# Kernel tuning notes

Measured on AMD Instinct MI355X. Metric: run time of the kernel, lower is better.

## Reference

```python
import jax, jax.numpy as jnp
import numpy as np

B, S, D = 16, 1, 2048
NH, NKV = 32, 8
HD = D // NH          # 64
GRP = NH // NKV       # 4
MAX_SEQ = 4096
START = MAX_SEQ - S   # 4095
HIDDEN = 5632         # 256*ceil((2*4*D/3)/256)
EPS = 1e-6


def _rope(x, cos, sin):
    # x: [b, s, h, d]; cos/sin: [s, d//2]; llama complex rotation on pairs
    b, s, h, d = x.shape
    xr = x.reshape(b, s, h, d // 2, 2)
    x0, x1 = xr[..., 0], xr[..., 1]
    c = cos[None, :, None, :]
    sn = sin[None, :, None, :]
    o0 = x0 * c - x1 * sn
    o1 = x0 * sn + x1 * c
    return jnp.stack([o0, o1], axis=-1).reshape(b, s, h, d)


def _rmsnorm(x, w, eps=EPS):
    return w * (x * jax.lax.rsqrt(jnp.mean(x * x, axis=-1, keepdims=True) + eps))


def setup_inputs() -> dict:
    key = jax.random.key(0)
    ks = jax.random.split(key, 12)
    sc = 0.02
    pos = jnp.arange(START, START + S, dtype=jnp.float32)
    inv = 1.0 / (10000.0 ** (jnp.arange(0, HD, 2, dtype=jnp.float32) / HD))
    ang = pos[:, None] * inv[None, :]  # [S, HD//2]
    return {
        "x": jax.random.normal(ks[0], (B, S, D), jnp.float32),
        "freqs_cos": jnp.cos(ang),
        "freqs_sin": jnp.sin(ang),
        "cache_k": jax.random.normal(ks[1], (B, MAX_SEQ, NKV, HD), jnp.float32),
        "cache_v": jax.random.normal(ks[2], (B, MAX_SEQ, NKV, HD), jnp.float32),
        "wq_w": jax.random.normal(ks[3], (D, D), jnp.float32) * sc,
        "wk_w": jax.random.normal(ks[4], (NKV * HD, D), jnp.float32) * sc,
        "wv_w": jax.random.normal(ks[5], (NKV * HD, D), jnp.float32) * sc,
        "wo_w": jax.random.normal(ks[6], (D, D), jnp.float32) * sc,
        "w1_w": jax.random.normal(ks[7], (HIDDEN, D), jnp.float32) * sc,
        "w2_w": jax.random.normal(ks[8], (D, HIDDEN), jnp.float32) * sc,
        "w3_w": jax.random.normal(ks[9], (D, D), jnp.float32) * sc,
        "attn_norm_w": jnp.ones((D,), jnp.float32),
        "ffn_norm_w": jnp.ones((D,), jnp.float32),
        "start_pos": START,
    }


def reference(x, freqs_cos, freqs_sin, cache_k, cache_v, wq_w, wk_w, wv_w, wo_w,
              w1_w, w2_w, w3_w, attn_norm_w, ffn_norm_w, start_pos):
    b, s, dim = x.shape
    # --- attention ---
    xn = _rmsnorm(x, attn_norm_w)
    xq = (xn @ wq_w.T).reshape(b, s, NH, HD)
    xk = (xn @ wk_w.T).reshape(b, s, NKV, HD)
    xv = (xn @ wv_w.T).reshape(b, s, NKV, HD)
    # source applies rotary embedding to q, k AND v
    xq = _rope(xq, freqs_cos, freqs_sin)
    xk = _rope(xk, freqs_cos, freqs_sin)
    xv = _rope(xv, freqs_cos, freqs_sin)
    # KV-cache write at start_pos, read prefix
    cache_k = jax.lax.dynamic_update_slice(cache_k, xk, (0, start_pos, 0, 0))
    cache_v = jax.lax.dynamic_update_slice(cache_v, xv, (0, start_pos, 0, 0))
    T = start_pos + s
    keys = cache_k[:, :T]   # [b, T, NKV, HD]
    vals = cache_v[:, :T]
    # GQA: group q heads per kv head (equivalent to repeat_kv + matmul)
    q = xq.reshape(b, s, NKV, GRP, HD)
    scores = jnp.einsum('bsKgd,btKd->bKgst', q, keys) / jnp.sqrt(jnp.float32(HD))
    probs = jax.nn.softmax(scores.astype(jnp.float32), axis=-1).astype(xq.dtype)
    attn = jnp.einsum('bKgst,btKd->bsKgd', probs, vals).reshape(b, s, dim)
    h = x + attn @ wo_w.T
    hn = _rmsnorm(h, ffn_norm_w)
    ff = jax.nn.silu(hn @ w1_w.T) @ w2_w.T + hn @ w3_w.T
    return h + ff
```

## Files before the change

### kernel.cpp

```cpp
#include <hip/hip_runtime.h>
#include <math.h>

#define NB      16
#define DIM     2048
#define NKVh    8
#define HDIM    64
#define GRP     4
#define MAXSEQ  4096
#define TPOS    4095
#define FFH     5632
#define NSPLIT  8
#define CHUNK   512

#define XN_OFF   0
#define Q_OFF    32768
#define ATTN_OFF 65536
#define H_OFF    98304
#define HN_OFF   131072
#define H1_OFF   163840
#define H3_OFF   253952
#define PML_OFF  286720
#define PO_OFF   294912

__device__ __forceinline__ float dot4(float4 a, float4 b) {
  return a.x * b.x + a.y * b.y + a.z * b.z + a.w * b.w;
}

__global__ __launch_bounds__(256) void rmsnorm_k(const float* __restrict__ x,
    const float* __restrict__ w, float* __restrict__ o) {
  int b = blockIdx.x;
  const float* xr = x + b * DIM;
  float ss = 0.f;
#pragma unroll
  for (int i = 0; i < DIM / 256; ++i) {
    float v = xr[threadIdx.x + i * 256];
    ss += v * v;
  }
#pragma unroll
  for (int m = 32; m >= 1; m >>= 1) ss += __shfl_xor(ss, m, 64);
  __shared__ float sred[4];
  if ((threadIdx.x & 63) == 0) sred[threadIdx.x >> 6] = ss;
  __syncthreads();
  float r = rsqrtf((sred[0] + sred[1] + sred[2] + sred[3]) * (1.f / DIM) + 1e-6f);
#pragma unroll
  for (int i = 0; i < DIM / 256; ++i) {
    int idx = threadIdx.x + i * 256;
    o[b * DIM + idx] = w[idx] * xr[idx] * r;
  }
}

template <int K4>
__device__ __forceinline__ float gemv64(const float* __restrict__ W,
                                        const float* __restrict__ X, int row0) {
  const int lane = threadIdx.x & 63;
  const float4* __restrict__ Wv = (const float4*)W;
  const float4* __restrict__ Xv = (const float4*)X;
  float a[64];
#pragma unroll
  for (int j = 0; j < 64; ++j) a[j] = 0.f;
#pragma unroll 2
  for (int it = 0; it < K4 / 64; ++it) {
    int k = it * 64 + lane;
    float4 w0 = Wv[(size_t)(row0 + 0) * K4 + k];
    float4 w1 = Wv[(size_t)(row0 + 1) * K4 + k];
    float4 w2 = Wv[(size_t)(row0 + 2) * K4 + k];
    float4 w3 = Wv[(size_t)(row0 + 3) * K4 + k];
#pragma unroll
    for (int b = 0; b < 16; ++b) {
      float4 xb = Xv[(size_t)b * K4 + k];
      a[0 * 16 + b] += dot4(w0, xb);
      a[1 * 16 + b] += dot4(w1, xb);
      a[2 * 16 + b] += dot4(w2, xb);
      a[3 * 16 + b] += dot4(w3, xb);
    }
  }
#pragma unroll
  for (int s = 0; s < 6; ++s) {
    const int m = 1 << s;
    const int mybit = (lane >> s) & 1;
#pragma unroll
    for (int i = 0; i < (64 >> (s + 1)); ++i) {
      float x0 = a[2 * i], x1 = a[2 * i + 1];
      float keep = mybit ? x1 : x0;
      float give = mybit ? x0 : x1;
      a[i] = keep + __shfl_xor(give, m, 64);
    }
  }
  return a[0];
}

__global__ __launch_bounds__(64) void qkv_k(const float* __restrict__ xn,
    const float* __restrict__ wq, const float* __restrict__ wk,
    const float* __restrict__ wv, const float* __restrict__ fc,
    const float* __restrict__ fs, float* __restrict__ qo,
    float* __restrict__ ck, float* __restrict__ cv) {
  int row0 = blockIdx.x * 4;
  const float* W;
  int lr, kind;
  if (row0 < DIM)            { W = wq; lr = row0;             kind = 0; }
  else if (row0 < DIM + 512) { W = wk; lr = row0 - DIM;       kind = 1; }
  else                       { W = wv; lr = row0 - DIM - 512; kind = 2; }
  float v = gemv64<512>(W, xn, lr);
  float pv = __shfl_xor(v, 16, 64);
  int lane = threadIdx.x & 63;
  int r = lane >> 4, b = lane & 15;
  int dl = (lr & 63) + r;
  int jp = ((lr & 63) + (r & 2)) >> 1;
  float c = fc[jp], sn = fs[jp];
  float o = (r & 1) ? (pv * sn + v * c) : (v * c - pv * sn);
  const float QS = 0.125f * 1.44269504088896f;
  if (kind == 0) {
    qo[b * DIM + lr + r] = o * QS;
  } else {
    int kvh = lr >> 6;
    float* cp = (kind == 1 ? ck : cv) +
                (((size_t)b * MAXSEQ + TPOS) * NKVh + kvh) * HDIM + dl;
    *cp = o;
  }
}

__global__ __launch_bounds__(256) void attn_part_k(const float* __restrict__ q,
    const float* __restrict__ ck, const float* __restrict__ cv,
    float* __restrict__ pml, float* __restrict__ po) {
  int blk = blockIdx.x;
  int sp = blk & (NSPLIT - 1);
  int bk = blk / NSPLIT;
  int kv = bk & 7, b = bk >> 3;
  int w = threadIdx.x >> 6, lane = threadIdx.x & 63;
  int t8 = lane >> 3, d8 = lane & 7;

  float4 q4[GRP][2];
#pragma unroll
  for (int g = 0; g < GRP; ++g) {
    const float* qp = q + b * DIM + (kv * GRP + g) * HDIM + d8 * 8;
    q4[g][0] = *(const float4*)qp;
    q4[g][1] = *(const float4*)(qp + 4);
  }

  float m[GRP], l[GRP];
  float4 o0[GRP], o1[GRP];
#pragma unroll
  for (int g = 0; g < GRP; ++g) {
    m[g] = -1e30f; l[g] = 0.f;
    o0[g] = make_float4(0.f, 0.f, 0.f, 0.f);
    o1[g] = make_float4(0.f, 0.f, 0.f, 0.f);
  }
  const size_t bkoff = ((size_t)b * MAXSEQ * NKVh + kv) * HDIM + d8 * 8;
  const float* Kp = ck + bkoff;
  const float* Vp = cv + bkoff;
  int tbase = sp * CHUNK + w * 128 + t8;
#pragma unroll 2
  for (int it = 0; it < 16; ++it) {
    size_t toff = (size_t)(tbase + it * 8) * (NKVh * HDIM);
    float4 ka = *(const float4*)(Kp + toff);
    float4 kb = *(const float4*)(Kp + toff + 4);
    float s[GRP];
#pragma unroll
    for (int g = 0; g < GRP; ++g)
      s[g] = dot4(ka, q4[g][0]) + dot4(kb, q4[g][1]);
#pragma unroll
    for (int msk = 1; msk < 8; msk <<= 1)
#pragma unroll
      for (int g = 0; g < GRP; ++g) s[g] += __shfl_xor(s[g], msk, 64);
    float4 va = *(const float4*)(Vp + toff);
    float4 vb = *(const float4*)(Vp + toff + 4);
#pragma unroll
    for (int g = 0; g < GRP; ++g) {
      float mn = fmaxf(m[g], s[g]);
      float sc = exp2f(m[g] - mn);
      float p  = exp2f(s[g] - mn);
      l[g] = l[g] * sc + p;
      o0[g].x = o0[g].x * sc + p * va.x;
      o0[g].y = o0[g].y * sc + p * va.y;
      o0[g].z = o0[g].z * sc + p * va.z;
      o0[g].w = o0[g].w * sc + p * va.w;
      o1[g].x = o1[g].x * sc + p * vb.x;
      o1[g].y = o1[g].y * sc + p * vb.y;
      o1[g].z = o1[g].z * sc + p * vb.z;
      o1[g].w = o1[g].w * sc + p * vb.w;
      m[g] = mn;
    }
  }
  __shared__ float sml[32][GRP][2];
  __shared__ float so[32][GRP][HDIM];
  int set = w * 8 + t8;
#pragma unroll
  for (int g = 0; g < GRP; ++g) {
    *(float4*)&so[set][g][d8 * 8]     = o0[g];
    *(float4*)&so[set][g][d8 * 8 + 4] = o1[g];
    if (d8 == 0) { sml[set][g][0] = m[g]; sml[set][g][1] = l[g]; }
  }
  __syncthreads();
  int g = threadIdx.x >> 6, d = threadIdx.x & 63;
  float M = -1e30f;
#pragma unroll
  for (int s2 = 0; s2 < 32; ++s2) M = fmaxf(M, sml[s2][g][0]);
  float L = 0.f, O = 0.f;
#pragma unroll
  for (int s2 = 0; s2 < 32; ++s2) {
    float e = exp2f(sml[s2][g][0] - M);
    L += e * sml[s2][g][1];
    O += e * so[s2][g][d];
  }
  int idx = (bk * GRP + g) * NSPLIT + sp;
  po[idx * HDIM + d] = O;
  if (d == 0) { pml[idx * 2] = M; pml[idx * 2 + 1] = L; }
}

__global__ __launch_bounds__(256) void attn_comb_k(const float* __restrict__ pml,
    const float* __restrict__ po, float* __restrict__ attn) {
  int t = blockIdx.x * 256 + threadIdx.x;
  int d = t & 63, bkg = t >> 6;
  float M = -1e30f;
#pragma unroll
  for (int sp = 0; sp < NSPLIT; ++sp) M = fmaxf(M, pml[(bkg * NSPLIT + sp) * 2]);
  float L = 0.f, O = 0.f;
#pragma unroll
  for (int sp = 0; sp < NSPLIT; ++sp) {
    float e = exp2f(pml[(bkg * NSPLIT + sp) * 2] - M);
    L += e * pml[(bkg * NSPLIT + sp) * 2 + 1];
    O += e * po[(bkg * NSPLIT + sp) * HDIM + d];
  }
  attn[bkg * HDIM + d] = O / L;
}

__global__ __launch_bounds__(64) void wo_k(const float* __restrict__ attn,
    const float* __restrict__ wo, const float* __restrict__ x,
    float* __restrict__ h) {
  int row0 = blockIdx.x * 4;
  float v = gemv64<512>(wo, attn, row0);
  int lane = threadIdx.x & 63;
  int r = lane >> 4, b = lane & 15;
  h[b * DIM + row0 + r] = x[b * DIM + row0 + r] + v;
}

__global__ __launch_bounds__(64) void ffn13_k(const float* __restrict__ hn,
    const float* __restrict__ w1, const float* __restrict__ w3,
    float* __restrict__ h1, float* __restrict__ h3) {
  int row0 = blockIdx.x * 4;
  bool is1 = row0 < FFH;
  const float* W = is1 ? w1 : w3;
  int lr = is1 ? row0 : row0 - FFH;
  float v = gemv64<512>(W, hn, lr);
  int lane = threadIdx.x & 63;
  int r = lane >> 4, b = lane & 15;
  if (is1) h1[b * FFH + lr + r] = v / (1.f + expf(-v));
  else     h3[b * DIM + lr + r] = v;
}

__global__ __launch_bounds__(64) void ffn2_k(const float* __restrict__ h1,
    const float* __restrict__ w2, const float* __restrict__ h,
    const float* __restrict__ h3, float* __restrict__ out) {
  int row0 = blockIdx.x * 4;
  float v = gemv64<1408>(w2, h1, row0);
  int lane = threadIdx.x & 63;
  int r = lane >> 4, b = lane & 15;
  out[b * DIM + row0 + r] = h[b * DIM + row0 + r] + h3[b * DIM + row0 + r] + v;
}

extern "C" void kernel_launch(void* const* d_in, const int* in_sizes, int n_in,
                              void* d_out, int out_size, void* d_ws, size_t ws_size,
                              hipStream_t stream) {
  (void)in_sizes; (void)n_in; (void)out_size; (void)ws_size;
  const float* x   = (const float*)d_in[0];
  const float* fc  = (const float*)d_in[1];
  const float* fs  = (const float*)d_in[2];
  float*       ck  = (float*)d_in[3];
  float*       cv  = (float*)d_in[4];
  const float* wq  = (const float*)d_in[5];
  const float* wk  = (const float*)d_in[6];
  const float* wvp = (const float*)d_in[7];
  const float* wo  = (const float*)d_in[8];
  const float* w1  = (const float*)d_in[9];
  const float* w2  = (const float*)d_in[10];
  const float* w3  = (const float*)d_in[11];
  const float* anw = (const float*)d_in[12];
  const float* fnw = (const float*)d_in[13];
  float* ws  = (float*)d_ws;
  float* out = (float*)d_out;

  rmsnorm_k<<<NB, 256, 0, stream>>>(x, anw, ws + XN_OFF);
  qkv_k<<<(DIM + 512 + 512) / 4, 64, 0, stream>>>(ws + XN_OFF, wq, wk, wvp, fc, fs,
                                                  ws + Q_OFF, ck, cv);
  attn_part_k<<<NB * NKVh * NSPLIT, 256, 0, stream>>>(ws + Q_OFF, ck, cv,
                                                      ws + PML_OFF, ws + PO_OFF);
  attn_comb_k<<<(NB * DIM) / 256, 256, 0, stream>>>(ws + PML_OFF, ws + PO_OFF, ws + ATTN_OFF);
  wo_k<<<DIM / 4, 64, 0, stream>>>(ws + ATTN_OFF, wo, x, ws + H_OFF);
  rmsnorm_k<<<NB, 256, 0, stream>>>(ws + H_OFF, fnw, ws + HN_OFF);
  ffn13_k<<<(FFH + DIM) / 4, 64, 0, stream>>>(ws + HN_OFF, w1, w3, ws + H1_OFF, ws + H3_OFF);
  ffn2_k<<<DIM / 4, 64, 0, stream>>>(ws + H1_OFF, w2, ws + H_OFF, ws + H3_OFF, out);
}
```

Measured before the change: 525.2 us.

## Pipeline KV tiles via global_load_lds and software-pipeline GEMV weight loads

Attention partial kernel now stages K/V tiles into LDS with direct global-to-LDS loads in a four-buffer ring, using an XOR-swizzled layout and explicit vmcnt waits and barriers. It also halves the number of splits, so each block covers 1024 positions. The GEMV helper double-buffers weight register loads across iterations and batches its X loads. The projection kernels now pack four waves per 256-thread block with a two-block occupancy hint. The aim is to hide memory latency in the bandwidth-bound attention and weight streaming, at the cost of more register pressure, fewer attention blocks and hand-written synchronization.

```diff
diff --git a/kernel.cpp b/kernel.cpp
--- a/kernel.cpp
+++ b/kernel.cpp
@@ -9,8 +9,8 @@
 #define MAXSEQ  4096
 #define TPOS    4095
 #define FFH     5632
-#define NSPLIT  8
-#define CHUNK   512
+#define NSPLIT  4
+#define CHUNK   1024
 
 #define XN_OFF   0
 #define Q_OFF    32768
@@ -26,6 +26,14 @@
   return a.x * b.x + a.y * b.y + a.z * b.z + a.w * b.w;
 }
 
+#define GLOAD_LDS(srcp, ldsp)                                                  \
+  __builtin_amdgcn_global_load_lds(                                            \
+      (const __attribute__((address_space(1))) void*)(srcp),                   \
+      (__attribute__((address_space(3))) void*)(ldsp), 16, 0, 0)
+
+#define WAITBAR(N) asm volatile("s_waitcnt vmcnt(" #N ")\n\ts_barrier" ::: "memory")
+#define RAWBAR()   asm volatile("s_barrier" ::: "memory")
+
 __global__ __launch_bounds__(256) void rmsnorm_k(const float* __restrict__ x,
     const float* __restrict__ w, float* __restrict__ o) {
   int b = blockIdx.x;
@@ -50,30 +58,41 @@
 }
 
 template <int K4>
-__device__ __forceinline__ float gemv64(const float* __restrict__ W,
-                                        const float* __restrict__ X, int row0) {
+__device__ __forceinline__ float gemv16(const float* __restrict__ W,
+                                        const float* __restrict__ X,
+                                        int row0) {
+  constexpr int NIT = K4 / 64;
   const int lane = threadIdx.x & 63;
   const float4* __restrict__ Wv = (const float4*)W;
   const float4* __restrict__ Xv = (const float4*)X;
   float a[64];
 #pragma unroll
   for (int j = 0; j < 64; ++j) a[j] = 0.f;
-#pragma unroll 2
-  for (int it = 0; it < K4 / 64; ++it) {
-    int k = it * 64 + lane;
-    float4 w0 = Wv[(size_t)(row0 + 0) * K4 + k];
-    float4 w1 = Wv[(size_t)(row0 + 1) * K4 + k];
-    float4 w2 = Wv[(size_t)(row0 + 2) * K4 + k];
-    float4 w3 = Wv[(size_t)(row0 + 3) * K4 + k];
-#pragma unroll
-    for (int b = 0; b < 16; ++b) {
-      float4 xb = Xv[(size_t)b * K4 + k];
-      a[0 * 16 + b] += dot4(w0, xb);
-      a[1 * 16 + b] += dot4(w1, xb);
-      a[2 * 16 + b] += dot4(w2, xb);
-      a[3 * 16 + b] += dot4(w3, xb);
-    }
-  }
+  float4 wa[4], wb[4];
+#define LDW(dst, it) { int kk = (it) * 64 + lane;                              \
+  _Pragma("unroll") for (int r = 0; r < 4; ++r)                                \
+    dst[r] = Wv[(size_t)(row0 + r) * K4 + kk]; }
+#define GST(wreg, it) { int kk = (it) * 64 + lane; float4 xx[16];              \
+  _Pragma("unroll") for (int bb = 0; bb < 16; ++bb)                            \
+    xx[bb] = Xv[(size_t)bb * K4 + kk];                                         \
+  _Pragma("unroll") for (int bb = 0; bb < 16; ++bb) {                          \
+    a[0 * 16 + bb] += dot4(wreg[0], xx[bb]);                                   \
+    a[1 * 16 + bb] += dot4(wreg[1], xx[bb]);                                   \
+    a[2 * 16 + bb] += dot4(wreg[2], xx[bb]);                                   \
+    a[3 * 16 + bb] += dot4(wreg[3], xx[bb]); } }
+  LDW(wa, 0);
+#pragma unroll 1
+  for (int it = 0; it < NIT - 2; it += 2) {
+    LDW(wb, it + 1);
+    GST(wa, it);
+    LDW(wa, it + 2);
+    GST(wb, it + 1);
+  }
+  LDW(wb, NIT - 1);
+  GST(wa, NIT - 2);
+  GST(wb, NIT - 1);
+#undef LDW
+#undef GST
 #pragma unroll
   for (int s = 0; s < 6; ++s) {
     const int m = 1 << s;
@@ -89,18 +108,20 @@
   return a[0];
 }
 
-__global__ __launch_bounds__(64) void qkv_k(const float* __restrict__ xn,
+__global__ __launch_bounds__(256, 2) void qkv_k(const float* __restrict__ xn,
     const float* __restrict__ wq, const float* __restrict__ wk,
     const float* __restrict__ wv, const float* __restrict__ fc,
     const float* __restrict__ fs, float* __restrict__ qo,
     float* __restrict__ ck, float* __restrict__ cv) {
-  int row0 = blockIdx.x * 4;
+  int rb = blockIdx.x * 16;
   const float* W;
-  int lr, kind;
-  if (row0 < DIM)            { W = wq; lr = row0;             kind = 0; }
-  else if (row0 < DIM + 512) { W = wk; lr = row0 - DIM;       kind = 1; }
-  else                       { W = wv; lr = row0 - DIM - 512; kind = 2; }
-  float v = gemv64<512>(W, xn, lr);
+  int lrb, kind;
+  if (rb < DIM)            { W = wq; lrb = rb;             kind = 0; }
+  else if (rb < DIM + 512) { W = wk; lrb = rb - DIM;       kind = 1; }
+  else                     { W = wv; lrb = rb - DIM - 512; kind = 2; }
+  int wv_ = threadIdx.x >> 6;
+  int lr = lrb + wv_ * 4;
+  float v = gemv16<512>(W, xn, lr);
   float pv = __shfl_xor(v, 16, 64);
   int lane = threadIdx.x & 63;
   int r = lane >> 4, b = lane & 15;
@@ -122,21 +143,29 @@
 __global__ __launch_bounds__(256) void attn_part_k(const float* __restrict__ q,
     const float* __restrict__ ck, const float* __restrict__ cv,
     float* __restrict__ pml, float* __restrict__ po) {
+  __shared__ float smem[16384];
   int blk = blockIdx.x;
   int sp = blk & (NSPLIT - 1);
-  int bk = blk / NSPLIT;
+  int bk = blk >> 2;
   int kv = bk & 7, b = bk >> 3;
-  int w = threadIdx.x >> 6, lane = threadIdx.x & 63;
+  int tid = threadIdx.x;
+  int w = tid >> 6, lane = tid & 63;
   int t8 = lane >> 3, d8 = lane & 7;
-
-  float4 q4[GRP][2];
+  int c0 = (d8 * 2) ^ t8, c1 = c0 ^ 1;
+  const int r4 = lane >> 4;
+  const int cps = lane & 15;
+
+  const size_t kvbase = ((size_t)b * MAXSEQ * NKVh + kv) * HDIM;
+  const float* Kpl = ck + kvbase;
+  const float* Vpl = cv + kvbase;
+
+  float4 q40[GRP], q41[GRP];
 #pragma unroll
   for (int g = 0; g < GRP; ++g) {
     const float* qp = q + b * DIM + (kv * GRP + g) * HDIM + d8 * 8;
-    q4[g][0] = *(const float4*)qp;
-    q4[g][1] = *(const float4*)(qp + 4);
-  }
-
+    q40[g] = *(const float4*)qp;
+    q41[g] = *(const float4*)(qp + 4);
+  }
   float m[GRP], l[GRP];
   float4 o0[GRP], o1[GRP];
 #pragma unroll
@@ -145,64 +174,90 @@
     o0[g] = make_float4(0.f, 0.f, 0.f, 0.f);
     o1[g] = make_float4(0.f, 0.f, 0.f, 0.f);
   }
-  const size_t bkoff = ((size_t)b * MAXSEQ * NKVh + kv) * HDIM + d8 * 8;
-  const float* Kp = ck + bkoff;
-  const float* Vp = cv + bkoff;
-  int tbase = sp * CHUNK + w * 128 + t8;
-#pragma unroll 2
-  for (int it = 0; it < 16; ++it) {
-    size_t toff = (size_t)(tbase + it * 8) * (NKVh * HDIM);
-    float4 ka = *(const float4*)(Kp + toff);
-    float4 kb = *(const float4*)(Kp + toff + 4);
-    float s[GRP];
-#pragma unroll
-    for (int g = 0; g < GRP; ++g)
-      s[g] = dot4(ka, q4[g][0]) + dot4(kb, q4[g][1]);
-#pragma unroll
-    for (int msk = 1; msk < 8; msk <<= 1)
-#pragma unroll
-      for (int g = 0; g < GRP; ++g) s[g] += __shfl_xor(s[g], msk, 64);
-    float4 va = *(const float4*)(Vp + toff);
-    float4 vb = *(const float4*)(Vp + toff + 4);
-#pragma unroll
-    for (int g = 0; g < GRP; ++g) {
-      float mn = fmaxf(m[g], s[g]);
-      float sc = exp2f(m[g] - mn);
-      float p  = exp2f(s[g] - mn);
-      l[g] = l[g] * sc + p;
-      o0[g].x = o0[g].x * sc + p * va.x;
-      o0[g].y = o0[g].y * sc + p * va.y;
-      o0[g].z = o0[g].z * sc + p * va.z;
-      o0[g].w = o0[g].w * sc + p * va.w;
-      o1[g].x = o1[g].x * sc + p * vb.x;
-      o1[g].y = o1[g].y * sc + p * vb.y;
-      o1[g].z = o1[g].z * sc + p * vb.z;
-      o1[g].w = o1[g].w * sc + p * vb.w;
-      m[g] = mn;
-    }
-  }
-  __shared__ float sml[32][GRP][2];
-  __shared__ float so[32][GRP][HDIM];
+  const int tg0 = sp * CHUNK;
+  const int sw0 = (cps ^ r4) * 4;
+  const int sw1 = (cps ^ (4 + r4)) * 4;
+
+#define STAGE(tile, bi) {                                                      \
+    int tbase = tg0 + (tile) * 32 + w * 8;                                     \
+    const float* Ks = Kpl + (size_t)tbase * (NKVh * HDIM);                     \
+    const float* Vs = Vpl + (size_t)tbase * (NKVh * HDIM);                     \
+    float* dK = smem + (bi) * 4096 + (w * 8) * 64;                             \
+    float* dV = dK + 2048;                                                     \
+    GLOAD_LDS(Ks + (size_t)r4 * 512 + sw0, dK);                                \
+    GLOAD_LDS(Ks + (size_t)(4 + r4) * 512 + sw1, dK + 256);                    \
+    GLOAD_LDS(Vs + (size_t)r4 * 512 + sw0, dV);                                \
+    GLOAD_LDS(Vs + (size_t)(4 + r4) * 512 + sw1, dV + 256); }
+
+#define COMPUTE(bi) {                                                          \
+    const float4* bK = (const float4*)(smem + (bi) * 4096);                    \
+    const float4* bV = bK + 512;                                               \
+    int base = (w * 8 + t8) * 16;                                              \
+    float4 ka = bK[base + c0], kb = bK[base + c1];                             \
+    float4 va = bV[base + c0], vb = bV[base + c1];                             \
+    float s_[GRP];                                                             \
+    _Pragma("unroll") for (int g = 0; g < GRP; ++g)                            \
+      s_[g] = dot4(ka, q40[g]) + dot4(kb, q41[g]);                             \
+    _Pragma("unroll") for (int msk = 1; msk < 8; msk <<= 1)                    \
+      _Pragma("unroll") for (int g = 0; g < GRP; ++g)                          \
+        s_[g] += __shfl_xor(s_[g], msk, 64);                                   \
+    _Pragma("unroll") for (int g = 0; g < GRP; ++g) {                          \
+      float mn = fmaxf(m[g], s_[g]);                                           \
+      float sc = exp2f(m[g] - mn);                                             \
+      float p  = exp2f(s_[g] - mn);                                            \
+      l[g] = l[g] * sc + p;                                                    \
+      o0[g].x = o0[g].x * sc + p * va.x;                                       \
+      o0[g].y = o0[g].y * sc + p * va.y;                                       \
+      o0[g].z = o0[g].z * sc + p * va.z;                                       \
+      o0[g].w = o0[g].w * sc + p * va.w;                                       \
+      o1[g].x = o1[g].x * sc + p * vb.x;                                       \
+      o1[g].y = o1[g].y * sc + p * vb.y;                                       \
+      o1[g].z = o1[g].z * sc + p * vb.z;                                       \
+      o1[g].w = o1[g].w * sc + p * vb.w;                                       \
+      m[g] = mn; } }
+
+#define STEPF(ti, bi, sbi) { STAGE((ti) + 2, sbi); WAITBAR(8); COMPUTE(bi); RAWBAR(); }
+
+  STAGE(0, 0);
+  STAGE(1, 1);
+#pragma unroll 1
+  for (int t = 0; t < 28; t += 4) {
+    STEPF(t + 0, 0, 2);
+    STEPF(t + 1, 1, 3);
+    STEPF(t + 2, 2, 0);
+    STEPF(t + 3, 3, 1);
+  }
+  STEPF(28, 0, 2);
+  STEPF(29, 1, 3);
+  { WAITBAR(4); COMPUTE(2); RAWBAR(); }
+  { WAITBAR(0); COMPUTE(3); }
+#undef STAGE
+#undef COMPUTE
+#undef STEPF
+
+  __syncthreads();
+  float* so  = smem;
+  float* sml = smem + 8192;
   int set = w * 8 + t8;
 #pragma unroll
   for (int g = 0; g < GRP; ++g) {
-    *(float4*)&so[set][g][d8 * 8]     = o0[g];
-    *(float4*)&so[set][g][d8 * 8 + 4] = o1[g];
-    if (d8 == 0) { sml[set][g][0] = m[g]; sml[set][g][1] = l[g]; }
+    *(float4*)&so[(set * GRP + g) * 64 + d8 * 8]     = o0[g];
+    *(float4*)&so[(set * GRP + g) * 64 + d8 * 8 + 4] = o1[g];
+    if (d8 == 0) { sml[(set * GRP + g) * 2] = m[g]; sml[(set * GRP + g) * 2 + 1] = l[g]; }
   }
   __syncthreads();
-  int g = threadIdx.x >> 6, d = threadIdx.x & 63;
+  int g2 = tid >> 6, d = tid & 63;
   float M = -1e30f;
 #pragma unroll
-  for (int s2 = 0; s2 < 32; ++s2) M = fmaxf(M, sml[s2][g][0]);
+  for (int s2 = 0; s2 < 32; ++s2) M = fmaxf(M, sml[(s2 * GRP + g2) * 2]);
   float L = 0.f, O = 0.f;
 #pragma unroll
   for (int s2 = 0; s2 < 32; ++s2) {
-    float e = exp2f(sml[s2][g][0] - M);
-    L += e * sml[s2][g][1];
-    O += e * so[s2][g][d];
-  }
-  int idx = (bk * GRP + g) * NSPLIT + sp;
+    float e = exp2f(sml[(s2 * GRP + g2) * 2] - M);
+    L += e * sml[(s2 * GRP + g2) * 2 + 1];
+    O += e * so[(s2 * GRP + g2) * 64 + d];
+  }
+  int idx = (bk * GRP + g2) * NSPLIT + sp;
   po[idx * HDIM + d] = O;
   if (d == 0) { pml[idx * 2] = M; pml[idx * 2 + 1] = L; }
 }
@@ -224,35 +279,35 @@
   attn[bkg * HDIM + d] = O / L;
 }
 
-__global__ __launch_bounds__(64) void wo_k(const float* __restrict__ attn,
+__global__ __launch_bounds__(256, 2) void wo_k(const float* __restrict__ attn,
     const float* __restrict__ wo, const float* __restrict__ x,
     float* __restrict__ h) {
-  int row0 = blockIdx.x * 4;
-  float v = gemv64<512>(wo, attn, row0);
+  int row0 = blockIdx.x * 16 + (threadIdx.x >> 6) * 4;
+  float v = gemv16<512>(wo, attn, row0);
   int lane = threadIdx.x & 63;
   int r = lane >> 4, b = lane & 15;
   h[b * DIM + row0 + r] = x[b * DIM + row0 + r] + v;
 }
 
-__global__ __launch_bounds__(64) void ffn13_k(const float* __restrict__ hn,
+__global__ __launch_bounds__(256, 2) void ffn13_k(const float* __restrict__ hn,
     const float* __restrict__ w1, const float* __restrict__ w3,
     float* __restrict__ h1, float* __restrict__ h3) {
-  int row0 = blockIdx.x * 4;
-  bool is1 = row0 < FFH;
+  int rb = blockIdx.x * 16;
+  bool is1 = rb < FFH;
   const float* W = is1 ? w1 : w3;
-  int lr = is1 ? row0 : row0 - FFH;
-  float v = gemv64<512>(W, hn, lr);
+  int lr = (is1 ? rb : rb - FFH) + (threadIdx.x >> 6) * 4;
+  float v = gemv16<512>(W, hn, lr);
   int lane = threadIdx.x & 63;
   int r = lane >> 4, b = lane & 15;
   if (is1) h1[b * FFH + lr + r] = v / (1.f + expf(-v));
   else     h3[b * DIM + lr + r] = v;
 }
 
-__global__ __launch_bounds__(64) void ffn2_k(const float* __restrict__ h1,
+__global__ __launch_bounds__(256, 2) void ffn2_k(const float* __restrict__ h1,
     const float* __restrict__ w2, const float* __restrict__ h,
     const float* __restrict__ h3, float* __restrict__ out) {
-  int row0 = blockIdx.x * 4;
-  float v = gemv64<1408>(w2, h1, row0);
+  int row0 = blockIdx.x * 16 + (threadIdx.x >> 6) * 4;
+  float v = gemv16<1408>(w2, h1, row0);
   int lane = threadIdx.x & 63;
   int r = lane >> 4, b = lane & 15;
   out[b * DIM + row0 + r] = h[b * DIM + row0 + r] + h3[b * DIM + row0 + r] + v;
@@ -280,13 +335,13 @@
   float* out = (float*)d_out;
 
   rmsnorm_k<<<NB, 256, 0, stream>>>(x, anw, ws + XN_OFF);
-  qkv_k<<<(DIM + 512 + 512) / 4, 64, 0, stream>>>(ws + XN_OFF, wq, wk, wvp, fc, fs,
-                                                  ws + Q_OFF, ck, cv);
+  qkv_k<<<(DIM + 512 + 512) / 16, 256, 0, stream>>>(ws + XN_OFF, wq, wk, wvp, fc, fs,
+                                                    ws + Q_OFF, ck, cv);
   attn_part_k<<<NB * NKVh * NSPLIT, 256, 0, stream>>>(ws + Q_OFF, ck, cv,
                                                       ws + PML_OFF, ws + PO_OFF);
   attn_comb_k<<<(NB * DIM) / 256, 256, 0, stream>>>(ws + PML_OFF, ws + PO_OFF, ws + ATTN_OFF);
-  wo_k<<<DIM / 4, 64, 0, stream>>>(ws + ATTN_OFF, wo, x, ws + H_OFF);
+  wo_k<<<DIM / 16, 256, 0, stream>>>(ws + ATTN_OFF, wo, x, ws + H_OFF);
   rmsnorm_k<<<NB, 256, 0, stream>>>(ws + H_OFF, fnw, ws + HN_OFF);
-  ffn13_k<<<(FFH + DIM) / 4, 64, 0, stream>>>(ws + HN_OFF, w1, w3, ws + H1_OFF, ws + H3_OFF);
-  ffn2_k<<<DIM / 4, 64, 0, stream>>>(ws + H1_OFF, w2, ws + H_OFF, ws + H3_OFF, out);
-}
+  ffn13_k<<<(FFH + DIM) / 16, 256, 0, stream>>>(ws + HN_OFF, w1, w3, ws + H1_OFF, ws + H3_OFF);
+  ffn2_k<<<DIM / 16, 256, 0, stream>>>(ws + H1_OFF, w2, ws + H_OFF, ws + H3_OFF, out);
+}
```

Measured after the change: 524.7 us. Within noise of the previous version (-0.1%).
